# Performance work log

Measured on AMD Instinct MI355X. Metric: run time of the kernel, lower is better.

Reference implementation:

```python
import jax, jax.numpy as jnp
import numpy as np

N, D_IN, H, OUT, L = 6144, 512, 512, 256, 3
EPS = 1e-5


def setup_inputs() -> dict:
    key = jax.random.key(0)
    ks = jax.random.split(key, 32)
    inp = {}
    inp["X"] = jax.random.normal(ks[0], (N, D_IN), dtype=jnp.float32)
    inp["adj"] = jax.random.randint(ks[1], (N, N), 0, 2).astype(jnp.float32)
    inp["adj_glo"] = jax.random.randint(ks[2], (N, N), 0, 2).astype(jnp.float32)
    s = 1.0 / np.sqrt(H)
    # projection + its BN
    inp["Wp"] = jax.random.normal(ks[3], (H, D_IN), dtype=jnp.float32) / np.sqrt(D_IN)
    inp["bp"] = jnp.zeros((H,), jnp.float32)
    inp["gp"] = jnp.ones((H,), jnp.float32)
    inp["betap"] = jnp.zeros((H,), jnp.float32)
    # per-layer params; layers 0,1 output H, layer 2 outputs OUT
    outs = [H, H, OUT]
    for i in range(L):
        o = outs[i]
        k = jax.random.split(ks[4 + i], 6)
        inp[f"Wq{i}"] = jax.random.normal(k[0], (H, H), jnp.float32) * s
        inp[f"Wk{i}"] = jax.random.normal(k[1], (H, H), jnp.float32) * s
        inp[f"Wv{i}"] = jax.random.normal(k[2], (H, H), jnp.float32) * s
        inp[f"Wo{i}"] = jax.random.normal(k[3], (o, H), jnp.float32) * s
        inp[f"bo{i}"] = jnp.zeros((o,), jnp.float32)
        inp[f"g{i}"] = jnp.ones((o,), jnp.float32)
        inp[f"beta{i}"] = jnp.zeros((o,), jnp.float32)
    return inp


def _normalize_adj(a):
    # symmetric GCN normalization D^{-1/2} A D^{-1/2}
    d = a.sum(axis=1)
    dis = jnp.where(d > 0, jax.lax.rsqrt(jnp.maximum(d, 1e-12)), 0.0)
    return a * dis[:, None] * dis[None, :]


def _bn(x, g, b):
    # BatchNorm1d, training mode: batch stats, biased variance
    m = x.mean(axis=0)
    v = x.var(axis=0)
    return g * (x - m) * jax.lax.rsqrt(v + EPS) + b


def _attn(h, adj, Wq, Wk, Wv, Wo, bo):
    Q = h @ Wq.T
    K = h @ Wk.T
    V = h @ Wv.T
    scores = (Q @ K.T) / np.sqrt(H)            # [N, N]
    scores = jnp.where(adj == 0, -jnp.inf, scores)
    attn = jax.nn.softmax(scores, axis=-1)
    return (attn @ V) @ Wo.T + bo


def reference(X, adj, adj_glo, Wp, bp, gp, betap,
              Wq0, Wk0, Wv0, Wo0, bo0, g0, beta0,
              Wq1, Wk1, Wv1, Wo1, bo1, g1, beta1,
              Wq2, Wk2, Wv2, Wo2, bo2, g2, beta2):
    # embedding: normalized global adjacency aggregation + projection + BN
    h = _normalize_adj(adj_glo) @ X
    h = h @ Wp.T + bp
    h = _bn(h, gp, betap)
    embed_features = h
    layers = [
        (Wq0, Wk0, Wv0, Wo0, bo0, g0, beta0),
        (Wq1, Wk1, Wv1, Wo1, bo1, g1, beta1),
        (Wq2, Wk2, Wv2, Wo2, bo2, g2, beta2),
    ]
    for i, (Wq, Wk, Wv, Wo, bo, g, b) in enumerate(layers):
        h_s = h
        h = _attn(h, adj, Wq, Wk, Wv, Wo, bo)
        h = jax.nn.relu(_bn(h, g, b))
        if i != L - 1:
            h = h + h_s
    return h, embed_features
```

## Files before the change

### kernel.cpp

```cpp
#include <hip/hip_runtime.h>
#include <cstdint>

#define NROW 6144
#define HDIM 512
#define DOUT 256
#define NEG_INF (-__builtin_inff())

typedef _Float16 half8 __attribute__((ext_vector_type(8)));
typedef _Float16 half4v __attribute__((ext_vector_type(4)));
typedef float f32x4 __attribute__((ext_vector_type(4)));

__device__ __forceinline__ void gld_lds16(void* lds, const void* g) {
  __builtin_amdgcn_global_load_lds(
      (const __attribute__((address_space(1))) void*)g,
      (__attribute__((address_space(3))) void*)lds, 16, 0, 0);
}

__global__ __launch_bounds__(256)
void gemm_f16(const _Float16* __restrict__ A, int lda,
              const _Float16* __restrict__ B, int ldb,
              float* __restrict__ Cf, _Float16* __restrict__ Ch, int ldc,
              int Kc, _Float16* __restrict__ Pk, long MN)
{
  __shared__ _Float16 As[128][32];
  __shared__ _Float16 Bs[128][32];
  const int tid = threadIdx.x;
  const int wave = tid >> 6, lane = tid & 63;
  const int wr = wave >> 1, wc = wave & 1;
  const int row0 = blockIdx.x * 128, col0 = blockIdx.y * 128;
  const int kbase = blockIdx.z * Kc;

  const int sr = lane >> 2;
  const int sk = ((lane & 3) ^ ((lane >> 3) & 3)) * 8;

  f32x4 acc[4][4];
  const f32x4 vzero = {0.f, 0.f, 0.f, 0.f};
  #pragma unroll
  for (int i = 0; i < 4; ++i)
    #pragma unroll
    for (int j = 0; j < 4; ++j)
      acc[i][j] = vzero;

  const int fr = lane & 15;
  const int fk = (((lane >> 4) ^ ((fr >> 1) & 3))) * 8;

  for (int k0 = kbase; k0 < kbase + Kc; k0 += 32) {
    #pragma unroll
    for (int c = 0; c < 2; ++c) {
      int rbase = c * 64 + wave * 16;
      gld_lds16(&As[rbase][0], A + (size_t)(row0 + rbase + sr) * lda + k0 + sk);
      gld_lds16(&Bs[rbase][0], B + (size_t)(col0 + rbase + sr) * ldb + k0 + sk);
    }
    __syncthreads();
    half8 af[4], bf[4];
    #pragma unroll
    for (int i = 0; i < 4; ++i)
      af[i] = *(const half8*)&As[wr * 64 + i * 16 + fr][fk];
    #pragma unroll
    for (int j = 0; j < 4; ++j)
      bf[j] = *(const half8*)&Bs[wc * 64 + j * 16 + fr][fk];
    #pragma unroll
    for (int i = 0; i < 4; ++i)
      #pragma unroll
      for (int j = 0; j < 4; ++j)
        acc[i][j] = __builtin_amdgcn_mfma_f32_16x16x32_f16(af[i], bf[j], acc[i][j], 0, 0, 0);
    __syncthreads();
  }

  const int lr = (lane >> 4) * 4;
  const int lc = lane & 15;
  if (Pk) {
    _Float16* dst = Pk + (size_t)blockIdx.z * MN;
    #pragma unroll
    for (int i = 0; i < 4; ++i)
      #pragma unroll
      for (int j = 0; j < 4; ++j)
        #pragma unroll
        for (int r = 0; r < 4; ++r) {
          int row = row0 + wr * 64 + i * 16 + lr + r;
          int col = col0 + wc * 64 + j * 16 + lc;
          dst[(size_t)row * ldc + col] = (_Float16)acc[i][j][r];
        }
    return;
  }
  #pragma unroll
  for (int i = 0; i < 4; ++i)
    #pragma unroll
    for (int j = 0; j < 4; ++j)
      #pragma unroll
      for (int r = 0; r < 4; ++r) {
        int row = row0 + wr * 64 + i * 16 + lr + r;
        int col = col0 + wc * 64 + j * 16 + lc;
        float v = acc[i][j][r];
        if (Cf) Cf[(size_t)row * ldc + col] = v;
        if (Ch) Ch[(size_t)row * ldc + col] = (_Float16)v;
      }
}

__global__ __launch_bounds__(256)
void reduce_splitk(const _Float16* __restrict__ Pk, long MN, int S, int cshift,
                   const float* __restrict__ rowscale,
                   float* __restrict__ Yf, _Float16* __restrict__ Yh)
{
  long n4 = MN >> 2;
  for (long i = (long)blockIdx.x * 256 + threadIdx.x; i < n4; i += (long)gridDim.x * 256) {
    float s0 = 0, s1 = 0, s2 = 0, s3 = 0;
    for (int z = 0; z < S; ++z) {
      half4v p = ((const half4v*)(Pk + (size_t)z * MN))[i];
      s0 += (float)p[0]; s1 += (float)p[1]; s2 += (float)p[2]; s3 += (float)p[3];
    }
    if (rowscale) {
      float sc = rowscale[(i * 4) >> cshift];
      s0 *= sc; s1 *= sc; s2 *= sc; s3 *= sc;
    }
    if (Yf) {
      float4 o; o.x = s0; o.y = s1; o.z = s2; o.w = s3;
      ((float4*)Yf)[i] = o;
    }
    if (Yh) {
      half4v o;
      o[0] = (_Float16)s0; o[1] = (_Float16)s1; o[2] = (_Float16)s2; o[3] = (_Float16)s3;
      ((half4v*)Yh)[i] = o;
    }
  }
}

__global__ __launch_bounds__(256)
void degree_convert(const float* __restrict__ A, _Float16* __restrict__ Ah,
                    float* __restrict__ dis)
{
  const int row = blockIdx.x;
  const float* a = A + (size_t)row * NROW;
  _Float16* o = Ah + (size_t)row * NROW;
  float s = 0.f;
  #pragma unroll
  for (int it = 0; it < 6; ++it) {
    int j = it * 1024 + threadIdx.x * 4;
    float4 v = *(const float4*)&a[j];
    s += v.x + v.y + v.z + v.w;
    half4v h;
    h[0] = (_Float16)v.x; h[1] = (_Float16)v.y; h[2] = (_Float16)v.z; h[3] = (_Float16)v.w;
    *(half4v*)&o[j] = h;
  }
  #pragma unroll
  for (int off = 32; off; off >>= 1) s += __shfl_xor(s, off);
  __shared__ float red[4];
  if ((threadIdx.x & 63) == 0) red[threadIdx.x >> 6] = s;
  __syncthreads();
  if (threadIdx.x == 0) {
    float d = red[0] + red[1] + red[2] + red[3];
    dis[row] = (d > 0.f) ? rsqrtf(fmaxf(d, 1e-12f)) : 0.f;
  }
}

__global__ __launch_bounds__(192)
void build_mask(const float* __restrict__ adj, uint32_t* __restrict__ bits)
{
  const int row = blockIdx.x;
  const int w = threadIdx.x;
  const float* a = adj + (size_t)row * NROW + w * 32;
  uint32_t m = 0;
  #pragma unroll
  for (int q = 0; q < 8; ++q) {
    float4 x = *(const float4*)&a[q * 4];
    m |= (x.x != 0.f ? 1u : 0u) << (q * 4 + 0);
    m |= (x.y != 0.f ? 1u : 0u) << (q * 4 + 1);
    m |= (x.z != 0.f ? 1u : 0u) << (q * 4 + 2);
    m |= (x.w != 0.f ? 1u : 0u) << (q * 4 + 3);
  }
  bits[(size_t)row * 192 + w] = m;
}

__global__ __launch_bounds__(256)
void convert_f16(const float* __restrict__ x, _Float16* __restrict__ y, float scale, long n4)
{
  for (long i = (long)blockIdx.x * 256 + threadIdx.x; i < n4; i += (long)gridDim.x * 256) {
    float4 v = ((const float4*)x)[i];
    half4v o;
    o[0] = (_Float16)(v.x * scale);
    o[1] = (_Float16)(v.y * scale);
    o[2] = (_Float16)(v.z * scale);
    o[3] = (_Float16)(v.w * scale);
    ((half4v*)y)[i] = o;
  }
}

__global__ __launch_bounds__(256)
void transpose_scale_f16(const float* __restrict__ src, const float* __restrict__ rowscale,
                         _Float16* __restrict__ dst, int R, int C)
{
  __shared__ _Float16 tile[64][72];
  const int c0 = blockIdx.x * 64, r0 = blockIdx.y * 64;
  const int tx4 = (threadIdx.x & 15) * 4, ty = threadIdx.x >> 4;
  #pragma unroll
  for (int p = 0; p < 4; ++p) {
    int r = p * 16 + ty;
    float4 v = *(const float4*)&src[(size_t)(r0 + r) * C + c0 + tx4];
    float sc = rowscale ? rowscale[r0 + r] : 1.0f;
    tile[tx4 + 0][r] = (_Float16)(v.x * sc);
    tile[tx4 + 1][r] = (_Float16)(v.y * sc);
    tile[tx4 + 2][r] = (_Float16)(v.z * sc);
    tile[tx4 + 3][r] = (_Float16)(v.w * sc);
  }
  __syncthreads();
  #pragma unroll
  for (int p = 0; p < 4; ++p) {
    int c = p * 16 + ty;
    half4v o;
    o[0] = tile[c][tx4 + 0];
    o[1] = tile[c][tx4 + 1];
    o[2] = tile[c][tx4 + 2];
    o[3] = tile[c][tx4 + 3];
    *(half4v*)&dst[(size_t)(c0 + c) * R + r0 + tx4] = o;
  }
}

__global__ __launch_bounds__(256)
void transpose_f16(const _Float16* __restrict__ src, int ld,
                   _Float16* __restrict__ dst, int R, int C)
{
  __shared__ _Float16 tile[64][72];
  const int c0 = blockIdx.x * 64, r0 = blockIdx.y * 64;
  const int tx4 = (threadIdx.x & 15) * 4, ty = threadIdx.x >> 4;
  #pragma unroll
  for (int p = 0; p < 4; ++p) {
    int r = p * 16 + ty;
    half4v v = *(const half4v*)&src[(size_t)(r0 + r) * ld + c0 + tx4];
    tile[tx4 + 0][r] = v[0];
    tile[tx4 + 1][r] = v[1];
    tile[tx4 + 2][r] = v[2];
    tile[tx4 + 3][r] = v[3];
  }
  __syncthreads();
  #pragma unroll
  for (int p = 0; p < 4; ++p) {
    int c = p * 16 + ty;
    half4v o;
    o[0] = tile[c][tx4 + 0];
    o[1] = tile[c][tx4 + 1];
    o[2] = tile[c][tx4 + 2];
    o[3] = tile[c][tx4 + 3];
    *(half4v*)&dst[(size_t)(c0 + c) * R + r0 + tx4] = o;
  }
}

__global__ __launch_bounds__(256)
void softmax_mask16(_Float16* __restrict__ Sf, const uint32_t* __restrict__ bits,
                    float* __restrict__ linv)
{
  const int row = blockIdx.x;
  _Float16* s = Sf + (size_t)row * NROW;
  const uint32_t* b = bits + (size_t)row * 192;
  const int tid = threadIdx.x;
  float v[24];
  float m = NEG_INF;
  #pragma unroll
  for (int it = 0; it < 3; ++it) {
    int j = it * 2048 + tid * 8;
    half8 sv = *(const half8*)&s[j];
    uint32_t w = (b[j >> 5] >> (j & 31)) & 0xffu;
    #pragma unroll
    for (int e = 0; e < 8; ++e) {
      float x = ((w >> e) & 1u) ? (float)sv[e] : NEG_INF;
      v[it * 8 + e] = x;
      m = fmaxf(m, x);
    }
  }
  #pragma unroll
  for (int off = 32; off; off >>= 1) m = fmaxf(m, __shfl_xor(m, off));
  __shared__ float red[4];
  const int lane = tid & 63, wave = tid >> 6;
  if (lane == 0) red[wave] = m;
  __syncthreads();
  m = fmaxf(fmaxf(red[0], red[1]), fmaxf(red[2], red[3]));
  __syncthreads();
  float l = 0.f;
  #pragma unroll
  for (int k = 0; k < 24; ++k) {
    float e = (v[k] == NEG_INF) ? 0.f : __expf(v[k] - m);
    v[k] = e; l += e;
  }
  #pragma unroll
  for (int off = 32; off; off >>= 1) l += __shfl_xor(l, off);
  if (lane == 0) red[wave] = l;
  __syncthreads();
  l = red[0] + red[1] + red[2] + red[3];
  if (tid == 0) linv[row] = (l > 0.f) ? (1.f / l) : 0.f;
  #pragma unroll
  for (int it = 0; it < 3; ++it) {
    int j = it * 2048 + tid * 8;
    half8 o;
    #pragma unroll
    for (int e = 0; e < 8; ++e) o[e] = (_Float16)v[it * 8 + e];
    *(half8*)&s[j] = o;
  }
}

__global__ __launch_bounds__(256)
void bn_partial(const float* __restrict__ X, int C,
                float* __restrict__ psum, float* __restrict__ psq)
{
  const int b = blockIdx.x;
  const int tid = threadIdx.x;
  const float* x = X + (size_t)b * 128 * C;
  float s0 = 0, q0 = 0, s1 = 0, q1 = 0;
  for (int r = 0; r < 128; ++r) {
    float a = x[(size_t)r * C + tid];
    s0 += a; q0 += a * a;
    if (C == 512) {
      float c2 = x[(size_t)r * C + tid + 256];
      s1 += c2; q1 += c2 * c2;
    }
  }
  psum[b * C + tid] = s0; psq[b * C + tid] = q0;
  if (C == 512) { psum[b * C + tid + 256] = s1; psq[b * C + tid + 256] = q1; }
}

__global__ void bn_finalize(const float* __restrict__ psum, const float* __restrict__ psq,
                            int C, const float* __restrict__ g, const float* __restrict__ beta,
                            float* __restrict__ scale, float* __restrict__ shift)
{
  int c = threadIdx.x + blockIdx.x * blockDim.x;
  if (c >= C) return;
  float s = 0, q = 0;
  for (int b = 0; b < 48; ++b) { s += psum[b * C + c]; q += psq[b * C + c]; }
  const float invN = 1.0f / 6144.0f;
  float mean = s * invN;
  float var = q * invN - mean * mean;
  float rstd = rsqrtf(fmaxf(var, 0.f) + 1e-5f);
  float sc = g[c] * rstd;
  scale[c] = sc;
  shift[c] = beta[c] - mean * sc;
}

__global__ __launch_bounds__(256)
void bn_apply(const float* __restrict__ X, const float* __restrict__ scale,
              const float* __restrict__ shift, const _Float16* __restrict__ residual,
              float* __restrict__ Yf, _Float16* __restrict__ Yh,
              int Cmask, long total, int do_relu)
{
  for (long i = (long)blockIdx.x * 256 + threadIdx.x; i < total; i += (long)gridDim.x * 256) {
    int c = (int)(i & Cmask);
    float v = X[i] * scale[c] + shift[c];
    if (do_relu) v = fmaxf(v, 0.f);
    if (residual) v += (float)residual[i];
    if (Yf) Yf[i] = v;
    if (Yh) Yh[i] = (_Float16)v;
  }
}

extern "C" void kernel_launch(void* const* d_in, const int* in_sizes, int n_in,
                              void* d_out, int out_size, void* d_ws, size_t ws_size,
                              hipStream_t stream)
{
  (void)in_sizes; (void)n_in; (void)out_size; (void)ws_size;
  const float* X     = (const float*)d_in[0];
  const float* adj   = (const float*)d_in[1];
  const float* adjg  = (const float*)d_in[2];
  const float* Wp    = (const float*)d_in[3];
  const float* gp    = (const float*)d_in[5];
  const float* betap = (const float*)d_in[6];

  float* out_h     = (float*)d_out;
  float* out_embed = out_h + (size_t)NROW * DOUT;

  char* base = (char*)d_ws;
  size_t off = 0;
  auto alloc = [&](size_t bytes) -> void* {
    void* p = base + off;
    off += (bytes + 255) & ~(size_t)255;
    return p;
  };

  const long MN512 = (long)NROW * 512;

  _Float16* Ag  = (_Float16*)alloc((size_t)NROW * NROW * 2);
  _Float16* Sf  = Ag;
  uint32_t* bits = (uint32_t*)alloc((size_t)NROW * 192 * 4);
  _Float16* Pk  = (_Float16*)alloc((size_t)8 * MN512 * 2);
  _Float16* XsT = (_Float16*)alloc((size_t)HDIM * NROW * 2);
  _Float16* Yh16 = (_Float16*)alloc((size_t)NROW * HDIM * 2);
  _Float16* Wph = (_Float16*)alloc((size_t)HDIM * HDIM * 2);
  _Float16* QKVW[3];
  for (int i = 0; i < 3; ++i) QKVW[i] = (_Float16*)alloc((size_t)1536 * HDIM * 2);
  _Float16* Woh[3];
  Woh[0] = (_Float16*)alloc((size_t)512 * 512 * 2);
  Woh[1] = (_Float16*)alloc((size_t)512 * 512 * 2);
  Woh[2] = (_Float16*)alloc((size_t)256 * 512 * 2);
  _Float16* QKVh = (_Float16*)alloc((size_t)NROW * 1536 * 2);
  _Float16* VTh  = (_Float16*)alloc((size_t)HDIM * NROW * 2);
  _Float16* AVh  = (_Float16*)alloc((size_t)NROW * HDIM * 2);
  float* xbuf = (float*)alloc((size_t)NROW * HDIM * 4);
  _Float16* hb16A = (_Float16*)alloc((size_t)NROW * HDIM * 2);
  _Float16* hb16B = (_Float16*)alloc((size_t)NROW * HDIM * 2);
  float* dis  = (float*)alloc((size_t)NROW * 4);
  float* linv = (float*)alloc((size_t)NROW * 4);
  float* psum = (float*)alloc((size_t)48 * 512 * 4);
  float* psq  = (float*)alloc((size_t)48 * 512 * 4);
  float* bnsc = (float*)alloc(512 * 4);
  float* bnsh = (float*)alloc(512 * 4);

  const float qk_scale = 0.21022410381342863f;

  degree_convert<<<NROW, 256, 0, stream>>>(adjg, Ag, dis);
  build_mask<<<NROW, 192, 0, stream>>>(adj, bits);
  transpose_scale_f16<<<dim3(8, 96), 256, 0, stream>>>(X, dis, XsT, NROW, HDIM);
  convert_f16<<<128, 256, 0, stream>>>(Wp, Wph, 1.f, 512 * 512 / 4);
  for (int i = 0; i < 3; ++i) {
    const float* Wq = (const float*)d_in[7 + i * 7 + 0];
    const float* Wk = (const float*)d_in[7 + i * 7 + 1];
    const float* Wv = (const float*)d_in[7 + i * 7 + 2];
    const float* Wo = (const float*)d_in[7 + i * 7 + 3];
    int o = (i < 2) ? 512 : 256;
    convert_f16<<<128, 256, 0, stream>>>(Wq, QKVW[i], qk_scale, 512 * 512 / 4);
    convert_f16<<<128, 256, 0, stream>>>(Wk, QKVW[i] + 512 * 512, qk_scale, 512 * 512 / 4);
    convert_f16<<<128, 256, 0, stream>>>(Wv, QKVW[i] + 2 * 512 * 512, 1.f, 512 * 512 / 4);
    convert_f16<<<128, 256, 0, stream>>>(Wo, Woh[i], 1.f, (long)o * 512 / 4);
  }

  gemm_f16<<<dim3(48, 4, 8), 256, 0, stream>>>(Ag, NROW, XsT, NROW, nullptr, nullptr, 512,
                                               768, Pk, MN512);
  reduce_splitk<<<1536, 256, 0, stream>>>(Pk, MN512, 8, 9, dis, nullptr, Yh16);
  gemm_f16<<<dim3(48, 4), 256, 0, stream>>>(Yh16, HDIM, Wph, HDIM, xbuf, nullptr, HDIM,
                                            512, nullptr, 0);
  bn_partial<<<48, 256, 0, stream>>>(xbuf, 512, psum, psq);
  bn_finalize<<<2, 256, 0, stream>>>(psum, psq, 512, gp, betap, bnsc, bnsh);
  bn_apply<<<2048, 256, 0, stream>>>(xbuf, bnsc, bnsh, nullptr, out_embed, hb16A,
                                     511, MN512, 0);

  _Float16* hbuf[2] = {hb16A, hb16B};
  int cur = 0;
  for (int i = 0; i < 3; ++i) {
    int o = (i < 2) ? 512 : 256;
    const float* gl = (const float*)d_in[7 + i * 7 + 5];
    const float* bl = (const float*)d_in[7 + i * 7 + 6];
    _Float16* hin = hbuf[cur];

    gemm_f16<<<dim3(48, 12), 256, 0, stream>>>(hin, HDIM, QKVW[i], HDIM, nullptr, QKVh, 1536,
                                               512, nullptr, 0);
    transpose_f16<<<dim3(8, 96), 256, 0, stream>>>(QKVh + 1024, 1536, VTh, NROW, HDIM);
    gemm_f16<<<dim3(48, 48), 256, 0, stream>>>(QKVh, 1536, QKVh + 512, 1536, nullptr, Sf, NROW,
                                               512, nullptr, 0);
    softmax_mask16<<<NROW, 256, 0, stream>>>(Sf, bits, linv);
    gemm_f16<<<dim3(48, 4, 8), 256, 0, stream>>>(Sf, NROW, VTh, NROW, nullptr, nullptr, 512,
                                                 768, Pk, MN512);
    reduce_splitk<<<1536, 256, 0, stream>>>(Pk, MN512, 8, 9, linv, nullptr, AVh);
    long MNo = (long)NROW * o;
    gemm_f16<<<dim3(48, o / 128, 4), 256, 0, stream>>>(AVh, HDIM, Woh[i], HDIM,
                                                       nullptr, nullptr, o, 128, Pk, MNo);
    reduce_splitk<<<1536, 256, 0, stream>>>(Pk, MNo, 4, (o == 512) ? 9 : 8, nullptr,
                                            xbuf, nullptr);
    bn_partial<<<48, 256, 0, stream>>>(xbuf, o, psum, psq);
    bn_finalize<<<2, 256, 0, stream>>>(psum, psq, o, gl, bl, bnsc, bnsh);
    if (i < 2) {
      bn_apply<<<2048, 256, 0, stream>>>(xbuf, bnsc, bnsh, hin, nullptr, hbuf[cur ^ 1],
                                         o - 1, (long)NROW * o, 1);
      cur ^= 1;
    } else {
      bn_apply<<<2048, 256, 0, stream>>>(xbuf, bnsc, bnsh, nullptr, out_h, nullptr,
                                         o - 1, (long)NROW * o, 1);
    }
  }
}
```

Baseline: 989.6 us.

## Add 256x256 double-buffered MFMA GEMM for large attention GEMMs, store pre-BN in fp16

Adds a new 512-thread GEMM kernel with 256x256 output tiles, double-buffered LDS filled by direct global-to-LDS loads, an XOR-swizzled LDS layout, a workgroup-order swizzle and raised wave priority around the MFMA block. It replaces the 128x128 kernel for the adjacency aggregation, the QK^T score GEMM and the attention-times-V GEMM, aiming for more data reuse per tile and fewer LDS and global loads per flop. It also stores the pre-BatchNorm activations in fp16 instead of fp32 to halve that memory traffic. The costs are higher register and LDS use, which lowers occupancy, and reduced precision for the batch statistics.

```diff
diff --git a/kernel.cpp b/kernel.cpp
--- a/kernel.cpp
+++ b/kernel.cpp
@@ -14,6 +14,122 @@
   __builtin_amdgcn_global_load_lds(
       (const __attribute__((address_space(1))) void*)g,
       (__attribute__((address_space(3))) void*)lds, 16, 0, 0);
+}
+
+__global__ __launch_bounds__(512)
+void gemm256(const _Float16* __restrict__ A, int lda,
+             const _Float16* __restrict__ B, int ldb,
+             _Float16* __restrict__ C, int ldc, int Kc, long MN)
+{
+  __shared__ _Float16 As[2][256][32];
+  __shared__ _Float16 Bs[2][256][32];
+  const int tid = threadIdx.x;
+  const int wave = tid >> 6, lane = tid & 63;
+  const int wr = wave >> 2, wc = wave & 3;
+
+  const int gx = gridDim.x, gy = gridDim.y;
+  const int nwg = gx * gy * gridDim.z;
+  int lin = (blockIdx.z * gy + blockIdx.y) * gx + blockIdx.x;
+  int swz = (nwg % 8 == 0) ? ((lin % 8) * (nwg >> 3) + (lin >> 3)) : lin;
+  const int bx = swz % gx;
+  const int by = (swz / gx) % gy;
+  const int bz = swz / (gx * gy);
+  const int row0 = bx * 256, col0 = by * 256;
+  const int kbase = bz * Kc;
+  const int nt = Kc >> 5;
+
+  const int g0 = wave * 64 + lane;
+  const int g1 = g0 + 512;
+  const int r0g = g0 >> 2, p0g = g0 & 3;
+  const int r1g = g1 >> 2, p1g = g1 & 3;
+  const size_t aoff0 = (size_t)(row0 + r0g) * lda + (p0g ^ ((r0g >> 1) & 3)) * 8;
+  const size_t aoff1 = (size_t)(row0 + r1g) * lda + (p1g ^ ((r1g >> 1) & 3)) * 8;
+  const size_t boff0 = (size_t)(col0 + r0g) * ldb + (p0g ^ ((r0g >> 1) & 3)) * 8;
+  const size_t boff1 = (size_t)(col0 + r1g) * ldb + (p1g ^ ((r1g >> 1) & 3)) * 8;
+  const int ldsh0 = (wave * 64) * 8;
+  const int ldsh1 = (512 + wave * 64) * 8;
+
+  f32x4 acc[8][4];
+  const f32x4 vzero = {0.f, 0.f, 0.f, 0.f};
+  #pragma unroll
+  for (int f = 0; f < 8; ++f)
+    #pragma unroll
+    for (int j = 0; j < 4; ++j)
+      acc[f][j] = vzero;
+
+  const int fr = lane & 15, sq = lane >> 4;
+
+  {
+    const _Float16* a = A + kbase;
+    const _Float16* b = B + kbase;
+    gld_lds16(&As[0][0][0] + ldsh0, a + aoff0);
+    gld_lds16(&As[0][0][0] + ldsh1, a + aoff1);
+    gld_lds16(&Bs[0][0][0] + ldsh0, b + boff0);
+    gld_lds16(&Bs[0][0][0] + ldsh1, b + boff1);
+    gld_lds16(&As[1][0][0] + ldsh0, a + 32 + aoff0);
+    gld_lds16(&As[1][0][0] + ldsh1, a + 32 + aoff1);
+    gld_lds16(&Bs[1][0][0] + ldsh0, b + 32 + boff0);
+    gld_lds16(&Bs[1][0][0] + ldsh1, b + 32 + boff1);
+  }
+  asm volatile("s_waitcnt vmcnt(4)" ::: "memory");
+  __builtin_amdgcn_s_barrier();
+  asm volatile("" ::: "memory");
+
+  for (int t = 0; t < nt; ++t) {
+    const int buf = t & 1;
+    half8 bfr[4];
+    #pragma unroll
+    for (int j = 0; j < 4; ++j) {
+      int r = wc * 64 + j * 16 + fr;
+      bfr[j] = *(const half8*)&Bs[buf][r][(sq ^ ((r >> 1) & 3)) * 8];
+    }
+    #pragma unroll
+    for (int mh = 0; mh < 2; ++mh) {
+      half8 afr[4];
+      #pragma unroll
+      for (int i = 0; i < 4; ++i) {
+        int r = wr * 128 + mh * 64 + i * 16 + fr;
+        afr[i] = *(const half8*)&As[buf][r][(sq ^ ((r >> 1) & 3)) * 8];
+      }
+      __builtin_amdgcn_s_setprio(1);
+      #pragma unroll
+      for (int i = 0; i < 4; ++i)
+        #pragma unroll
+        for (int j = 0; j < 4; ++j)
+          acc[mh * 4 + i][j] =
+              __builtin_amdgcn_mfma_f32_16x16x32_f16(afr[i], bfr[j], acc[mh * 4 + i][j], 0, 0, 0);
+      __builtin_amdgcn_s_setprio(0);
+    }
+    if (t + 1 < nt) {
+      asm volatile("s_waitcnt lgkmcnt(0)" ::: "memory");
+      __builtin_amdgcn_s_barrier();
+      if (t + 2 < nt) {
+        const _Float16* a = A + kbase + (t + 2) * 32;
+        const _Float16* b = B + kbase + (t + 2) * 32;
+        gld_lds16(&As[buf][0][0] + ldsh0, a + aoff0);
+        gld_lds16(&As[buf][0][0] + ldsh1, a + aoff1);
+        gld_lds16(&Bs[buf][0][0] + ldsh0, b + boff0);
+        gld_lds16(&Bs[buf][0][0] + ldsh1, b + boff1);
+        asm volatile("s_waitcnt vmcnt(4)" ::: "memory");
+      } else {
+        asm volatile("s_waitcnt vmcnt(0)" ::: "memory");
+      }
+      __builtin_amdgcn_s_barrier();
+      asm volatile("" ::: "memory");
+    }
+  }
+
+  _Float16* dst = C + (size_t)bz * MN;
+  #pragma unroll
+  for (int f = 0; f < 8; ++f)
+    #pragma unroll
+    for (int j = 0; j < 4; ++j)
+      #pragma unroll
+      for (int r = 0; r < 4; ++r) {
+        int row = row0 + wr * 128 + f * 16 + sq * 4 + r;
+        int col = col0 + wc * 64 + j * 16 + fr;
+        dst[(size_t)row * ldc + col] = (_Float16)acc[f][j][r];
+      }
 }
 
 __global__ __launch_bounds__(256)
@@ -297,18 +413,18 @@
 }
 
 __global__ __launch_bounds__(256)
-void bn_partial(const float* __restrict__ X, int C,
+void bn_partial(const _Float16* __restrict__ X, int C,
                 float* __restrict__ psum, float* __restrict__ psq)
 {
   const int b = blockIdx.x;
   const int tid = threadIdx.x;
-  const float* x = X + (size_t)b * 128 * C;
+  const _Float16* x = X + (size_t)b * 128 * C;
   float s0 = 0, q0 = 0, s1 = 0, q1 = 0;
   for (int r = 0; r < 128; ++r) {
-    float a = x[(size_t)r * C + tid];
+    float a = (float)x[(size_t)r * C + tid];
     s0 += a; q0 += a * a;
     if (C == 512) {
-      float c2 = x[(size_t)r * C + tid + 256];
+      float c2 = (float)x[(size_t)r * C + tid + 256];
       s1 += c2; q1 += c2 * c2;
     }
   }
@@ -334,14 +450,14 @@
 }
 
 __global__ __launch_bounds__(256)
-void bn_apply(const float* __restrict__ X, const float* __restrict__ scale,
+void bn_apply(const _Float16* __restrict__ X, const float* __restrict__ scale,
               const float* __restrict__ shift, const _Float16* __restrict__ residual,
               float* __restrict__ Yf, _Float16* __restrict__ Yh,
               int Cmask, long total, int do_relu)
 {
   for (long i = (long)blockIdx.x * 256 + threadIdx.x; i < total; i += (long)gridDim.x * 256) {
     int c = (int)(i & Cmask);
-    float v = X[i] * scale[c] + shift[c];
+    float v = (float)X[i] * scale[c] + shift[c];
     if (do_relu) v = fmaxf(v, 0.f);
     if (residual) v += (float)residual[i];
     if (Yf) Yf[i] = v;
@@ -390,7 +506,7 @@
   _Float16* QKVh = (_Float16*)alloc((size_t)NROW * 1536 * 2);
   _Float16* VTh  = (_Float16*)alloc((size_t)HDIM * NROW * 2);
   _Float16* AVh  = (_Float16*)alloc((size_t)NROW * HDIM * 2);
-  float* xbuf = (float*)alloc((size_t)NROW * HDIM * 4);
+  _Float16* xh   = (_Float16*)alloc((size_t)NROW * HDIM * 2);
   _Float16* hb16A = (_Float16*)alloc((size_t)NROW * HDIM * 2);
   _Float16* hb16B = (_Float16*)alloc((size_t)NROW * HDIM * 2);
   float* dis  = (float*)alloc((size_t)NROW * 4);
@@ -418,14 +534,13 @@
     convert_f16<<<128, 256, 0, stream>>>(Wo, Woh[i], 1.f, (long)o * 512 / 4);
   }
 
-  gemm_f16<<<dim3(48, 4, 8), 256, 0, stream>>>(Ag, NROW, XsT, NROW, nullptr, nullptr, 512,
-                                               768, Pk, MN512);
+  gemm256<<<dim3(24, 2, 8), 512, 0, stream>>>(Ag, NROW, XsT, NROW, Pk, 512, 768, MN512);
   reduce_splitk<<<1536, 256, 0, stream>>>(Pk, MN512, 8, 9, dis, nullptr, Yh16);
-  gemm_f16<<<dim3(48, 4), 256, 0, stream>>>(Yh16, HDIM, Wph, HDIM, xbuf, nullptr, HDIM,
+  gemm_f16<<<dim3(48, 4), 256, 0, stream>>>(Yh16, HDIM, Wph, HDIM, nullptr, xh, HDIM,
                                             512, nullptr, 0);
-  bn_partial<<<48, 256, 0, stream>>>(xbuf, 512, psum, psq);
+  bn_partial<<<48, 256, 0, stream>>>(xh, 512, psum, psq);
   bn_finalize<<<2, 256, 0, stream>>>(psum, psq, 512, gp, betap, bnsc, bnsh);
-  bn_apply<<<2048, 256, 0, stream>>>(xbuf, bnsc, bnsh, nullptr, out_embed, hb16A,
+  bn_apply<<<2048, 256, 0, stream>>>(xh, bnsc, bnsh, nullptr, out_embed, hb16A,
                                      511, MN512, 0);
 
   _Float16* hbuf[2] = {hb16A, hb16B};
@@ -439,25 +554,23 @@
     gemm_f16<<<dim3(48, 12), 256, 0, stream>>>(hin, HDIM, QKVW[i], HDIM, nullptr, QKVh, 1536,
                                                512, nullptr, 0);
     transpose_f16<<<dim3(8, 96), 256, 0, stream>>>(QKVh + 1024, 1536, VTh, NROW, HDIM);
-    gemm_f16<<<dim3(48, 48), 256, 0, stream>>>(QKVh, 1536, QKVh + 512, 1536, nullptr, Sf, NROW,
-                                               512, nullptr, 0);
+    gemm256<<<dim3(24, 24), 512, 0, stream>>>(QKVh, 1536, QKVh + 512, 1536, Sf, NROW, 512, 0);
     softmax_mask16<<<NROW, 256, 0, stream>>>(Sf, bits, linv);
-    gemm_f16<<<dim3(48, 4, 8), 256, 0, stream>>>(Sf, NROW, VTh, NROW, nullptr, nullptr, 512,
-                                                 768, Pk, MN512);
+    gemm256<<<dim3(24, 2, 8), 512, 0, stream>>>(Sf, NROW, VTh, NROW, Pk, 512, 768, MN512);
     reduce_splitk<<<1536, 256, 0, stream>>>(Pk, MN512, 8, 9, linv, nullptr, AVh);
     long MNo = (long)NROW * o;
     gemm_f16<<<dim3(48, o / 128, 4), 256, 0, stream>>>(AVh, HDIM, Woh[i], HDIM,
                                                        nullptr, nullptr, o, 128, Pk, MNo);
     reduce_splitk<<<1536, 256, 0, stream>>>(Pk, MNo, 4, (o == 512) ? 9 : 8, nullptr,
-                                            xbuf, nullptr);
-    bn_partial<<<48, 256, 0, stream>>>(xbuf, o, psum, psq);
+                                            nullptr, xh);
+    bn_partial<<<48, 256, 0, stream>>>(xh, o, psum, psq);
     bn_finalize<<<2, 256, 0, stream>>>(psum, psq, o, gl, bl, bnsc, bnsh);
     if (i < 2) {
-      bn_apply<<<2048, 256, 0, stream>>>(xbuf, bnsc, bnsh, hin, nullptr, hbuf[cur ^ 1],
+      bn_apply<<<2048, 256, 0, stream>>>(xh, bnsc, bnsh, hin, nullptr, hbuf[cur ^ 1],
                                          o - 1, (long)NROW * o, 1);
       cur ^= 1;
     } else {
-      bn_apply<<<2048, 256, 0, stream>>>(xbuf, bnsc, bnsh, nullptr, out_h, nullptr,
+      bn_apply<<<2048, 256, 0, stream>>>(xh, bnsc, bnsh, nullptr, out_h, nullptr,
                                          o - 1, (long)NROW * o, 1);
     }
   }
```

Measured after the change: 1.035 ms. 1.05x slower.
